# Performance work log

Hardware: AMD Instinct MI355X
Metric: run time of the kernel (lower is better)

The kernel has to match this reference:

```python
import jax, jax.numpy as jnp
import numpy as np

B, L, D, H, A = 4, 2048, 1024, 16, 64  # batch, seq, d_model, n_head, d_head


def setup_inputs() -> dict:
    key = jax.random.key(0)
    ks = jax.random.split(key, 6)
    scale = 1.0 / np.sqrt(D)
    return {
        "xq": jax.random.normal(ks[0], (B, L, D), dtype=jnp.float32),
        "xkv": jax.random.normal(ks[1], (B, L, D), dtype=jnp.float32),
        "Q": jax.random.normal(ks[2], (D, H, A), dtype=jnp.float32) * scale,
        "K": jax.random.normal(ks[3], (D, H, A), dtype=jnp.float32) * scale,
        "V": jax.random.normal(ks[4], (D, H, A), dtype=jnp.float32) * scale,
        "O": jax.random.normal(ks[5], (D, H, A), dtype=jnp.float32) * scale,
    }


def reference(xq, xkv, Q, K, V, O):
    # embed: 'dha, ...ld -> ...lha'
    q = jnp.einsum('dha,bld->blha', Q, xq)
    k = jnp.einsum('dha,bld->blha', K, xkv)
    v = jnp.einsum('dha,bld->blha', V, xkv)
    # outer: '...lha, ...mha -> ...hlm'  (full LxL score matrix, no scaling in source)
    scores = jnp.einsum('blha,bmha->bhlm', q, k)
    attn = jax.nn.softmax(scores, axis=-1)  # dropout p=0 (eval)
    # score: '...hlm, ...mha -> ...lha'
    ctx = jnp.einsum('bhlm,bmha->blha', attn, v)
    # output: '...dha, ...lha -> ...ld'
    return jnp.einsum('dha,blha->bld', O, ctx)
```

## Files before the change

kernel.cpp:

```cpp
#include <hip/hip_runtime.h>
#include <math.h>

typedef __bf16 bf16;
typedef bf16 bf16x8 __attribute__((ext_vector_type(8)));
typedef bf16 bf16x4 __attribute__((ext_vector_type(4)));
typedef float f32x4 __attribute__((ext_vector_type(4)));
typedef float f32x16 __attribute__((ext_vector_type(16)));

#define B_ 4
#define L_ 2048
#define D_ 1024
#define H_ 16
#define A_ 64
#define HA_ 1024
#define BL_ 8192
#define LOG2E 1.44269504088896340736f

__device__ __forceinline__ void gload16(const void* g, void* l) {
  __builtin_amdgcn_global_load_lds((const __attribute__((address_space(1))) void*)g,
                                   (__attribute__((address_space(3))) void*)l,
                                   16, 0, 0);
}

__device__ __forceinline__ unsigned cvt_pk_bf16(float lo, float hi) {
  unsigned r;
  asm volatile("v_cvt_pk_bf16_f32 %0, %1, %2" : "=v"(r) : "v"(lo), "v"(hi));
  return r;
}

__device__ __forceinline__ void permswap(unsigned& a, unsigned& b) {
  asm volatile("v_permlane32_swap_b32 %0, %1" : "+v"(a), "+v"(b));
}

__global__ __launch_bounds__(256) void cast_all(const float* __restrict__ xq,
                                                const float* __restrict__ xkv,
                                                const float* __restrict__ ow,
                                                bf16* __restrict__ xq_b,
                                                bf16* __restrict__ xkv_b,
                                                bf16* __restrict__ wo_b) {
  const int NX = BL_ * D_ / 8;
  const int NW = D_ * HA_ / 8;
  int i = blockIdx.x * blockDim.x + threadIdx.x;
  const float* src;
  bf16* dst;
  int j;
  if (i < NX) { src = xq; dst = xq_b; j = i; }
  else if (i < 2 * NX) { src = xkv; dst = xkv_b; j = i - NX; }
  else if (i < 2 * NX + NW) { src = ow; dst = wo_b; j = i - 2 * NX; }
  else return;
  const float4* s = reinterpret_cast<const float4*>(src) + (size_t)j * 2;
  float4 a = s[0], b = s[1];
  bf16x8 o;
  o[0] = (bf16)a.x; o[1] = (bf16)a.y; o[2] = (bf16)a.z; o[3] = (bf16)a.w;
  o[4] = (bf16)b.x; o[5] = (bf16)b.y; o[6] = (bf16)b.z; o[7] = (bf16)b.w;
  *reinterpret_cast<bf16x8*>(dst + (size_t)j * 8) = o;
}

__global__ __launch_bounds__(256) void transpose_cast_w3(const float* __restrict__ wq,
                                                         const float* __restrict__ wk,
                                                         const float* __restrict__ wv,
                                                         bf16* __restrict__ oq,
                                                         bf16* __restrict__ ok,
                                                         bf16* __restrict__ ov) {
  __shared__ float tile[32][33];
  const int z = blockIdx.z;
  const float* w = (z == 0) ? wq : (z == 1) ? wk : wv;
  bf16* wt = (z == 0) ? oq : (z == 1) ? ok : ov;
  const float scale = (z == 0) ? LOG2E : 1.0f;
  const int d0 = blockIdx.y * 32, h0 = blockIdx.x * 32;
  const int tx = threadIdx.x, ty = threadIdx.y;
  #pragma unroll
  for (int j = 0; j < 4; j++)
    tile[ty + j * 8][tx] = w[(size_t)(d0 + ty + j * 8) * HA_ + h0 + tx];
  __syncthreads();
  #pragma unroll
  for (int j = 0; j < 4; j++)
    wt[(size_t)(h0 + ty + j * 8) * D_ + d0 + tx] = (bf16)(tile[tx][ty + j * 8] * scale);
}

template <int MODE>
__device__ __forceinline__ void gemm_bt_core(const bf16* __restrict__ Ap,
                                             const bf16* __restrict__ Bp,
                                             void* __restrict__ Cp,
                                             int m0, int n0) {
  const int K = 1024;
  __shared__ __align__(16) bf16 As[128 * 32];
  __shared__ __align__(16) bf16 Bs[128 * 32];
  const int tid = threadIdx.x;
  const int lane = tid & 63, w = tid >> 6;
  const int wr = w >> 1, wc = w & 1;
  const int g = lane >> 4, c = lane & 15;
  f32x4 acc[4][4] = {};
  const int srow = tid >> 2, sch = tid & 3;
  const int sw0 = (sch ^ (srow & 3)) * 8;
  for (int k0 = 0; k0 < K; k0 += 32) {
    gload16(Ap + (size_t)(m0 + srow) * K + k0 + sw0, As + tid * 8);
    gload16(Ap + (size_t)(m0 + 64 + srow) * K + k0 + sw0, As + (256 + tid) * 8);
    gload16(Bp + (size_t)(n0 + srow) * K + k0 + sw0, Bs + tid * 8);
    gload16(Bp + (size_t)(n0 + 64 + srow) * K + k0 + sw0, Bs + (256 + tid) * 8);
    __syncthreads();
    bf16x8 af[4], bfr[4];
    #pragma unroll
    for (int m = 0; m < 4; m++)
      af[m] = *reinterpret_cast<const bf16x8*>(As + (wr * 64 + m * 16 + c) * 32 + ((g ^ (c & 3)) * 8));
    #pragma unroll
    for (int n = 0; n < 4; n++)
      bfr[n] = *reinterpret_cast<const bf16x8*>(Bs + (wc * 64 + n * 16 + c) * 32 + ((g ^ (c & 3)) * 8));
    #pragma unroll
    for (int m = 0; m < 4; m++)
      #pragma unroll
      for (int n = 0; n < 4; n++)
        acc[m][n] = __builtin_amdgcn_mfma_f32_16x16x32_bf16(af[m], bfr[n], acc[m][n], 0, 0, 0);
    __syncthreads();
  }
  #pragma unroll
  for (int m = 0; m < 4; m++) {
    #pragma unroll
    for (int n = 0; n < 4; n++) {
      if (MODE == 2) {
        int row0 = m0 + wr * 64 + m * 16 + g * 4;
        int col = n0 + wc * 64 + n * 16 + c;
        int b = row0 >> 11, l0 = row0 & 2047, h = col >> 6, a = col & 63;
        bf16x4 o4;
        #pragma unroll
        for (int i = 0; i < 4; i++) o4[i] = (bf16)acc[m][n][i];
        *reinterpret_cast<bf16x4*>((bf16*)Cp + ((size_t)(b * H_ + h) * A_ + a) * L_ + l0) = o4;
      } else {
        #pragma unroll
        for (int i = 0; i < 4; i++) {
          int row = m0 + wr * 64 + m * 16 + g * 4 + i;
          int col = n0 + wc * 64 + n * 16 + c;
          float v = acc[m][n][i];
          if (MODE == 0) {
            int b = row >> 11, l = row & 2047, h = col >> 6, a = col & 63;
            ((bf16*)Cp)[(((size_t)b * H_ + h) * L_ + l) * A_ + a] = (bf16)v;
          } else {
            ((float*)Cp)[(size_t)row * 1024 + col] = v;
          }
        }
      }
    }
  }
}

__device__ __forceinline__ void xcd_mn(int id, int& m0, int& n0) {
  int xcd = id & 7, j = id >> 3;
  m0 = (xcd * 8 + (j >> 3)) * 128;
  n0 = (j & 7) * 128;
}

__global__ __launch_bounds__(256, 2) void gemm_proj(const bf16* xq_b, const bf16* xkv_b,
                                                    const bf16* wq, const bf16* wk, const bf16* wv,
                                                    bf16* qb, bf16* kb, bf16* vtb) {
  int m0, n0;
  xcd_mn(blockIdx.x, m0, n0);
  const int z = blockIdx.z;
  if (z == 0)      gemm_bt_core<0>(xq_b, wq, qb, m0, n0);
  else if (z == 1) gemm_bt_core<0>(xkv_b, wk, kb, m0, n0);
  else             gemm_bt_core<2>(xkv_b, wv, vtb, m0, n0);
}

__global__ __launch_bounds__(256, 2) void gemm_out_k(const bf16* ctx, const bf16* wo, float* out) {
  int m0, n0;
  xcd_mn(blockIdx.x, m0, n0);
  gemm_bt_core<1>(ctx, wo, out, m0, n0);
}

__device__ __forceinline__ void pa_build(const f32x16& s, bf16x8& f0, bf16x8& f1) {
  #pragma unroll
  for (int sl = 0; sl < 2; sl++) {
    unsigned a0 = cvt_pk_bf16(s[8 * sl + 0], s[8 * sl + 1]);
    unsigned b0 = cvt_pk_bf16(s[8 * sl + 4], s[8 * sl + 5]);
    permswap(a0, b0);
    unsigned a1 = cvt_pk_bf16(s[8 * sl + 2], s[8 * sl + 3]);
    unsigned b1 = cvt_pk_bf16(s[8 * sl + 6], s[8 * sl + 7]);
    permswap(a1, b1);
    uint4 v; v.x = a0; v.y = a1; v.z = b0; v.w = b1;
    if (sl == 0) f0 = __builtin_bit_cast(bf16x8, v);
    else         f1 = __builtin_bit_cast(bf16x8, v);
  }
}

__global__ __launch_bounds__(512, 2) void attn_kernel(const bf16* __restrict__ qg,
                                                      const bf16* __restrict__ kg,
                                                      const bf16* __restrict__ vtg,
                                                      bf16* __restrict__ ctx) {
  __shared__ __align__(16) bf16 Ks[4][64 * 64];
  __shared__ __align__(16) bf16 Vs[4][64 * 64];
  const int tid = threadIdx.x;
  const int lane = tid & 63;
  const int w = tid >> 6;
  const int c = lane & 31;
  const int hi = lane >> 5;
  const int cs7 = c & 7;
  const int bh = blockIdx.x;
  const int q0 = blockIdx.y * 256;
  const bf16* qh = qg + (size_t)bh * L_ * A_;
  const bf16* kh = kg + (size_t)bh * L_ * A_;
  const bf16* vh = vtg + (size_t)bh * A_ * L_;

  const int qrow = q0 + w * 32 + c;
  bf16x8 qf[4];
  #pragma unroll
  for (int ds = 0; ds < 4; ds++)
    qf[ds] = *reinterpret_cast<const bf16x8*>(qh + (size_t)qrow * A_ + ds * 16 + hi * 8);

  bf16x8 ones;
  #pragma unroll
  for (int j = 0; j < 8; j++) ones[j] = (bf16)1.0f;

  f32x16 oacc0 = {}, oacc1 = {};
  f32x16 ssum = {};

  int koA[4], koB[4];
  #pragma unroll
  for (int ds = 0; ds < 4; ds++) {
    koA[ds] = c * 64 + ((2 * ds + hi) ^ cs7) * 8;
    koB[ds] = (32 + c) * 64 + ((2 * ds + hi) ^ cs7) * 8;
  }

  const int sr = tid >> 3, sc = tid & 7;
  const int ss = (sc ^ (sr & 7)) * 8;
  const bf16* ksrc = kh + (size_t)sr * A_ + ss;
  const bf16* vsrc = vh + (size_t)sr * L_ + ss;

  auto stage = [&](int t) {
    int buf = t & 3;
    gload16(ksrc + (size_t)t * 4096, &Ks[buf][tid * 8]);
    gload16(vsrc + (size_t)t * 64, &Vs[buf][tid * 8]);
  };

  auto compute = [&](int t) {
    const bf16* Kc = Ks[t & 3];
    const bf16* Vc = Vs[t & 3];
    f32x16 s0 = {}, s1 = {};
    __builtin_amdgcn_s_setprio(1);
    #pragma unroll
    for (int ds = 0; ds < 4; ds++) {
      bf16x8 k0 = *reinterpret_cast<const bf16x8*>(Kc + koA[ds]);
      bf16x8 k1 = *reinterpret_cast<const bf16x8*>(Kc + koB[ds]);
      s0 = __builtin_amdgcn_mfma_f32_32x32x16_bf16(k0, qf[ds], s0, 0, 0, 0);
      s1 = __builtin_amdgcn_mfma_f32_32x32x16_bf16(k1, qf[ds], s1, 0, 0, 0);
    }
    __builtin_amdgcn_s_setprio(0);

    #pragma unroll
    for (int r = 0; r < 16; r++) {
      s0[r] = __builtin_amdgcn_exp2f(s0[r]);
      s1[r] = __builtin_amdgcn_exp2f(s1[r]);
    }

    bf16x8 paf0, paf1, paf2, paf3;
    pa_build(s0, paf0, paf1);
    pa_build(s1, paf2, paf3);

    __builtin_amdgcn_s_setprio(1);
    #pragma unroll
    for (int ks = 0; ks < 4; ks++) {
      const bf16x8 pa = (ks == 0) ? paf0 : (ks == 1) ? paf1 : (ks == 2) ? paf2 : paf3;
      bf16x8 v0 = *reinterpret_cast<const bf16x8*>(Vc + koA[ks]);
      bf16x8 v1 = *reinterpret_cast<const bf16x8*>(Vc + koB[ks]);
      oacc0 = __builtin_amdgcn_mfma_f32_32x32x16_bf16(v0, pa, oacc0, 0, 0, 0);
      oacc1 = __builtin_amdgcn_mfma_f32_32x32x16_bf16(v1, pa, oacc1, 0, 0, 0);
      ssum = __builtin_amdgcn_mfma_f32_32x32x16_bf16(ones, pa, ssum, 0, 0, 0);
    }
    __builtin_amdgcn_s_setprio(0);
  };

  stage(0);
  stage(1);
  __syncthreads();

  for (int p = 0; p < L_ / 128; p++) {
    int t0 = 2 * p;
    if (t0 + 2 < L_ / 64) {
      stage(t0 + 2);
      stage(t0 + 3);
    }
    compute(t0);
    compute(t0 + 1);
    __syncthreads();
  }

  float inv = 1.f / ssum[0];
  const int b = bh >> 4, h = bh & 15;
  bf16* crow = ctx + (((size_t)b * L_ + qrow) * H_ + h) * A_;
  #pragma unroll
  for (int n = 0; n < 2; n++) {
    #pragma unroll
    for (int rq = 0; rq < 4; rq++) {
      bf16x4 o4;
      #pragma unroll
      for (int j = 0; j < 4; j++) {
        float v = (n == 0) ? oacc0[rq * 4 + j] : oacc1[rq * 4 + j];
        o4[j] = (bf16)(v * inv);
      }
      *reinterpret_cast<bf16x4*>(crow + n * 32 + rq * 8 + hi * 4) = o4;
    }
  }
}

extern "C" void kernel_launch(void* const* d_in, const int* in_sizes, int n_in,
                              void* d_out, int out_size, void* d_ws, size_t ws_size,
                              hipStream_t stream) {
  const float* xq = (const float*)d_in[0];
  const float* xkv = (const float*)d_in[1];
  const float* Qw = (const float*)d_in[2];
  const float* Kw = (const float*)d_in[3];
  const float* Vw = (const float*)d_in[4];
  const float* Ow = (const float*)d_in[5];
  float* out = (float*)d_out;

  char* ws = (char*)d_ws;
  const size_t SZ16 = (size_t)BL_ * HA_ * sizeof(bf16);
  const size_t SZW = (size_t)D_ * HA_ * sizeof(bf16);
  bf16* xq_b = (bf16*)(ws);
  bf16* xkv_b = (bf16*)(ws + SZ16);
  bf16* wq_t = (bf16*)(ws + 2 * SZ16);
  bf16* wk_t = (bf16*)(ws + 2 * SZ16 + SZW);
  bf16* wv_t = (bf16*)(ws + 2 * SZ16 + 2 * SZW);
  bf16* wo_b = (bf16*)(ws + 2 * SZ16 + 3 * SZW);
  bf16* qb = (bf16*)(ws + 2 * SZ16 + 4 * SZW);
  bf16* kb = qb + (size_t)BL_ * HA_;
  bf16* vtb = kb + (size_t)BL_ * HA_;
  bf16* ctxb = xkv_b;

  const int NCAST = (2 * BL_ * D_ + D_ * HA_) / 8;
  cast_all<<<(NCAST + 255) / 256, 256, 0, stream>>>(xq, xkv, Ow, xq_b, xkv_b, wo_b);
  transpose_cast_w3<<<dim3(32, 32, 3), dim3(32, 8), 0, stream>>>(Qw, Kw, Vw, wq_t, wk_t, wv_t);

  gemm_proj<<<dim3(512, 1, 3), 256, 0, stream>>>(xq_b, xkv_b, wq_t, wk_t, wv_t, qb, kb, vtb);
  attn_kernel<<<dim3(64, 8), 512, 0, stream>>>(qb, kb, vtb, ctxb);
  gemm_out_k<<<512, 256, 0, stream>>>(ctxb, wo_b, out);
}
```

Baseline: 197.8 us.

## Shrink attention blocks to 256 threads with double-buffered K/V staging

The attention kernel now runs 4 waves per block covering 128 query rows instead of 8 waves covering 256, and the grid doubles to 1024 blocks. K/V staging moves from a 4-slot, two-tiles-per-barrier pipeline to a 2-slot double buffer with one barrier per 64-key tile, with each thread issuing two loads per tile. The aim is more resident blocks per CU and a smaller LDS footprint. The cost is twice as many barriers, a shallower prefetch, and K/V being reloaded by twice as many blocks.

```diff
diff --git a/kernel.cpp b/kernel.cpp
--- a/kernel.cpp
+++ b/kernel.cpp
@@ -181,12 +181,12 @@
   }
 }
 
-__global__ __launch_bounds__(512, 2) void attn_kernel(const bf16* __restrict__ qg,
+__global__ __launch_bounds__(256, 4) void attn_kernel(const bf16* __restrict__ qg,
                                                       const bf16* __restrict__ kg,
                                                       const bf16* __restrict__ vtg,
                                                       bf16* __restrict__ ctx) {
-  __shared__ __align__(16) bf16 Ks[4][64 * 64];
-  __shared__ __align__(16) bf16 Vs[4][64 * 64];
+  __shared__ __align__(16) bf16 Ks[2][64 * 64];
+  __shared__ __align__(16) bf16 Vs[2][64 * 64];
   const int tid = threadIdx.x;
   const int lane = tid & 63;
   const int w = tid >> 6;
@@ -194,7 +194,7 @@
   const int hi = lane >> 5;
   const int cs7 = c & 7;
   const int bh = blockIdx.x;
-  const int q0 = blockIdx.y * 256;
+  const int q0 = blockIdx.y * 128;
   const bf16* qh = qg + (size_t)bh * L_ * A_;
   const bf16* kh = kg + (size_t)bh * L_ * A_;
   const bf16* vh = vtg + (size_t)bh * A_ * L_;
@@ -221,18 +221,27 @@
 
   const int sr = tid >> 3, sc = tid & 7;
   const int ss = (sc ^ (sr & 7)) * 8;
-  const bf16* ksrc = kh + (size_t)sr * A_ + ss;
-  const bf16* vsrc = vh + (size_t)sr * L_ + ss;
-
-  auto stage = [&](int t) {
-    int buf = t & 3;
-    gload16(ksrc + (size_t)t * 4096, &Ks[buf][tid * 8]);
-    gload16(vsrc + (size_t)t * 64, &Vs[buf][tid * 8]);
+  const bf16* ksrc0 = kh + (size_t)sr * A_ + ss;
+  const bf16* ksrc1 = kh + (size_t)(sr + 32) * A_ + ss;
+  const bf16* vsrc0 = vh + (size_t)sr * L_ + ss;
+  const bf16* vsrc1 = vh + (size_t)(sr + 32) * L_ + ss;
+
+  auto stage = [&](int buf, int t) {
+    gload16(ksrc0 + (size_t)t * 4096, &Ks[buf][tid * 8]);
+    gload16(ksrc1 + (size_t)t * 4096, &Ks[buf][2048 + tid * 8]);
+    gload16(vsrc0 + (size_t)t * 64, &Vs[buf][tid * 8]);
+    gload16(vsrc1 + (size_t)t * 64, &Vs[buf][2048 + tid * 8]);
   };
 
-  auto compute = [&](int t) {
-    const bf16* Kc = Ks[t & 3];
-    const bf16* Vc = Vs[t & 3];
+  stage(0, 0);
+  __syncthreads();
+  int cur = 0;
+
+  for (int t = 0; t < L_ / 64; t++) {
+    if (t < L_ / 64 - 1) stage(cur ^ 1, t + 1);
+    const bf16* Kc = Ks[cur];
+    const bf16* Vc = Vs[cur];
+
     f32x16 s0 = {}, s1 = {};
     __builtin_amdgcn_s_setprio(1);
     #pragma unroll
@@ -265,21 +274,9 @@
       ssum = __builtin_amdgcn_mfma_f32_32x32x16_bf16(ones, pa, ssum, 0, 0, 0);
     }
     __builtin_amdgcn_s_setprio(0);
-  };
-
-  stage(0);
-  stage(1);
-  __syncthreads();
-
-  for (int p = 0; p < L_ / 128; p++) {
-    int t0 = 2 * p;
-    if (t0 + 2 < L_ / 64) {
-      stage(t0 + 2);
-      stage(t0 + 3);
-    }
-    compute(t0);
-    compute(t0 + 1);
+
     __syncthreads();
+    cur ^= 1;
   }
 
   float inv = 1.f / ssum[0];
@@ -330,6 +327,6 @@
   transpose_cast_w3<<<dim3(32, 32, 3), dim3(32, 8), 0, stream>>>(Qw, Kw, Vw, wq_t, wk_t, wv_t);
 
   gemm_proj<<<dim3(512, 1, 3), 256, 0, stream>>>(xq_b, xkv_b, wq_t, wk_t, wv_t, qb, kb, vtb);
-  attn_kernel<<<dim3(64, 8), 512, 0, stream>>>(qb, kb, vtb, ctxb);
+  attn_kernel<<<dim3(64, 16), 256, 0, stream>>>(qb, kb, vtb, ctxb);
   gemm_out_k<<<512, 256, 0, stream>>>(ctxb, wo_b, out);
 }
```

New measurement: 200.7 us. No clear change (+1.4%).
